# Performance work log

Hardware: AMD Instinct MI355X
Metric: run time of the kernel (lower is better)

## Reference

```python
import jax, jax.numpy as jnp
import numpy as np

D_MODEL = 256
D_STATE = 64
D_CONV = 4
EXPAND = 2
HEADDIM = 16
D_INNER = EXPAND * D_MODEL            # 512
NHEADS = D_INNER // HEADDIM           # 32
CONV_DIM = D_INNER + 2 * D_STATE      # 640 (ngroups=1)
D_IN_PROJ = 2 * D_INNER + 2 * D_STATE + NHEADS  # 1184
BATCH = 256
SEQ = 200


def _ln(x, g, b, eps=1e-12):
    m = jnp.mean(x, axis=-1, keepdims=True)
    v = jnp.mean((x - m) ** 2, axis=-1, keepdims=True)
    return (x - m) * jax.lax.rsqrt(v + eps) * g + b


def setup_inputs() -> dict:
    key = jax.random.key(0)
    ks = jax.random.split(key, 16)
    def gn(i, shape, s=0.02):
        return jax.random.normal(ks[i], shape, jnp.float32) * s
    return {
        "input_tensor": jax.random.normal(ks[0], (BATCH, SEQ, D_MODEL), jnp.float32),
        # Mamba2 params
        "in_proj_w": gn(1, (D_MODEL, D_IN_PROJ)),
        "conv_w": gn(2, (CONV_DIM, D_CONV), 0.1),
        "conv_b": jnp.zeros((CONV_DIM,), jnp.float32),
        "dt_bias": gn(3, (NHEADS,), 0.1),
        "A_log": jnp.log(jax.random.uniform(ks[4], (NHEADS,), jnp.float32, 1.0, 16.0)),
        "D_skip": jnp.ones((NHEADS,), jnp.float32),
        "rms_w": jnp.ones((D_INNER,), jnp.float32),
        "out_proj_w": gn(5, (D_INNER, D_MODEL)),
        # Layer norms / mixers
        "ln_g": jnp.ones((D_MODEL,), jnp.float32),
        "ln_b": jnp.zeros((D_MODEL,), jnp.float32),
        "filt_w": gn(6, (1, SEQ // 2 + 1, D_MODEL, 2), 0.02),
        "filt_ln_g": jnp.ones((D_MODEL,), jnp.float32),
        "filt_ln_b": jnp.zeros((D_MODEL,), jnp.float32),
        "alpha": jax.random.uniform(ks[7], (D_MODEL,), jnp.float32),
        "beta": jax.random.uniform(ks[8], (D_MODEL,), jnp.float32),
        # FFN
        "ffn_w1": gn(9, (D_MODEL, 4 * D_MODEL)),
        "ffn_b1": jnp.zeros((4 * D_MODEL,), jnp.float32),
        "ffn_w2": gn(10, (4 * D_MODEL, D_MODEL)),
        "ffn_b2": jnp.zeros((D_MODEL,), jnp.float32),
        "ffn_ln_g": jnp.ones((D_MODEL,), jnp.float32),
        "ffn_ln_b": jnp.zeros((D_MODEL,), jnp.float32),
    }


def _mamba2(x, in_proj_w, conv_w, conv_b, dt_bias, A_log, D_skip, rms_w, out_proj_w):
    b, l, _ = x.shape
    zxbcdt = x @ in_proj_w                                  # [b,l,1184]
    z, xBC, dt = jnp.split(zxbcdt, [D_INNER, D_INNER + CONV_DIM], axis=-1)
    # depthwise causal conv over time + SiLU
    xp = jnp.pad(xBC, ((0, 0), (D_CONV - 1, 0), (0, 0)))
    conv = conv_b + sum(conv_w[:, k] * xp[:, k:k + l, :] for k in range(D_CONV))
    xBC = jax.nn.silu(conv)
    xs, Bm, Cm = jnp.split(xBC, [D_INNER, D_INNER + D_STATE], axis=-1)
    xh = xs.reshape(b, l, NHEADS, HEADDIM)
    dt = jax.nn.softplus(dt + dt_bias)                      # [b,l,h]
    A = -jnp.exp(A_log)                                     # [h]
    dA = jnp.exp(dt * A)                                    # [b,l,h]
    dtx = dt[..., None] * xh                                # [b,l,h,p]

    def step(state, inp):
        dA_t, dtx_t, B_t, C_t = inp
        # state: [b,h,p,n]
        state = dA_t[:, :, None, None] * state + dtx_t[..., None] * B_t[:, None, None, :]
        y_t = jnp.einsum('bhpn,bn->bhp', state, C_t)
        return state, y_t

    state0 = jnp.zeros((b, NHEADS, HEADDIM, D_STATE), x.dtype)
    _, y = jax.lax.scan(step, state0,
                        (jnp.moveaxis(dA, 1, 0), jnp.moveaxis(dtx, 1, 0),
                         jnp.moveaxis(Bm, 1, 0), jnp.moveaxis(Cm, 1, 0)))
    y = jnp.moveaxis(y, 0, 1) + D_skip[None, None, :, None] * xh   # skip connection
    y = y.reshape(b, l, D_INNER)
    # gated RMSNorm: rmsnorm(y * silu(z)) * w
    g = y * jax.nn.silu(z)
    g = g * jax.lax.rsqrt(jnp.mean(g * g, axis=-1, keepdims=True) + 1e-5) * rms_w
    return g @ out_proj_w


def reference(input_tensor, in_proj_w, conv_w, conv_b, dt_bias, A_log, D_skip,
              rms_w, out_proj_w, ln_g, ln_b, filt_w, filt_ln_g, filt_ln_b,
              alpha, beta, ffn_w1, ffn_b1, ffn_w2, ffn_b2, ffn_ln_g, ffn_ln_b):
    x = input_tensor
    h1 = _mamba2(x, in_proj_w, conv_w, conv_b, dt_bias, A_log, D_skip, rms_w, out_proj_w)
    h1 = _ln(h1 + x, ln_g, ln_b)
    # FFT filter branch
    xf = jnp.fft.rfft(x, axis=1, norm='ortho')
    w = filt_w[..., 0] + 1j * filt_w[..., 1]                # [1,101,d]
    xi = jnp.fft.irfft(xf * w, n=SEQ, axis=1, norm='ortho').astype(x.dtype)
    h2 = _ln(xi + x, filt_ln_g, filt_ln_b)
    h = alpha * h1 + beta * h2
    hid = jax.nn.gelu(h @ ffn_w1 + ffn_b1, approximate=False) @ ffn_w2 + ffn_b2
    return _ln(hid + h, ffn_ln_g, ffn_ln_b)
```

## Files before the change

### kernel.cpp

```cpp
#include <hip/hip_runtime.h>
#include <math.h>

#define BATCHN 256
#define SEQ 200
#define DMODEL 256
#define DINNER 512
#define NH 32
#define HD 16
#define DSTATE 64
#define DINPROJ 1184
#define XBCLD 672
#define BL (BATCHN*SEQ)
#define NF 101
#define NJ 202
#define NJP 208
#define XBASE 655360
#define TC 25
#define NCH 8

typedef __attribute__((ext_vector_type(8))) short bf16x8;
typedef __attribute__((ext_vector_type(4))) float f32x4;

__device__ inline unsigned short f2bf(float f) {
    union { float f; unsigned u; } v; v.f = f;
    unsigned r = v.u + 0x7FFFu + ((v.u >> 16) & 1u);
    return (unsigned short)(r >> 16);
}
__device__ inline float bf2f(unsigned short h) {
    union { unsigned u; float f; } v; v.u = ((unsigned)h) << 16;
    return v.f;
}

#define GLOAD16(src, dst) __builtin_amdgcn_global_load_lds( \
    (const __attribute__((address_space(1))) void*)(src),   \
    (__attribute__((address_space(3))) void*)(dst), 16, 0, 0)

__global__ void init_dft_kernel(unsigned short* __restrict__ EF, unsigned short* __restrict__ EI)
{
    const float ang = 6.28318530717958647692f / 200.0f;
    int idx = blockIdx.x * 256 + threadIdx.x;
    if (idx < NJ * SEQ) {
        int f = idx / SEQ, t = idx - f * SEQ;
        float v;
        if (f <= 100) { int ph = (f * t) % 200; v = cosf(ang * (float)ph); }
        else { int ff = f - 101; int ph = (ff * t) % 200; v = -sinf(ang * (float)ph); }
        EF[idx] = f2bf(v);
    } else if (idx < NJ * SEQ + SEQ * NJP) {
        int j2 = idx - NJ * SEQ;
        int t = j2 / NJP, j = j2 - t * NJP;
        float v;
        if (j == 0) v = 1.0f / 200.0f;
        else if (j == 100) v = ((t & 1) ? -1.0f : 1.0f) / 200.0f;
        else if (j < 100) { int ph = (j * t) % 200; v = 2.0f * cosf(ang * (float)ph) / 200.0f; }
        else if (j >= 202 || j == 101 || j == 201) v = 0.0f;
        else { int f = j - 101; int ph = (f * t) % 200; v = -2.0f * sinf(ang * (float)ph) / 200.0f; }
        EI[j2] = f2bf(v);
    }
}

__global__ void pack_wT_kernel(const float* __restrict__ src, unsigned short* __restrict__ dst,
                               int srcld, int coloff, int N, int K)
{
    int idx = blockIdx.x * 256 + threadIdx.x;
    if (idx >= N * K) return;
    int n = idx / K, k = idx - n * K;
    dst[idx] = f2bf(src[(long long)k * srcld + coloff + n]);
}

__global__ void f2bf_kernel(const float* __restrict__ X, unsigned short* __restrict__ O)
{
    long long i = ((long long)blockIdx.x * 256 + threadIdx.x) * 8;
    float4 a = ((const float4*)(X + i))[0];
    float4 b = ((const float4*)(X + i))[1];
    uint4 o;
    o.x = (unsigned)f2bf(a.x) | ((unsigned)f2bf(a.y) << 16);
    o.y = (unsigned)f2bf(a.z) | ((unsigned)f2bf(a.w) << 16);
    o.z = (unsigned)f2bf(b.x) | ((unsigned)f2bf(b.y) << 16);
    o.w = (unsigned)f2bf(b.z) | ((unsigned)f2bf(b.w) << 16);
    *(uint4*)(O + i) = o;
}

__global__ void xT_kernel(const float* __restrict__ X, unsigned short* __restrict__ XT)
{
    __shared__ float tile[32][33];
    int b = blockIdx.z, t0 = blockIdx.x * 32, d0 = blockIdx.y * 32;
    int tx = threadIdx.x & 31, ty = threadIdx.x >> 5;
    const float* xb = X + (long long)b * SEQ * DMODEL;
#pragma unroll
    for (int i = 0; i < 4; i++) {
        int t = t0 + ty + i * 8;
        tile[ty + i * 8][tx] = (t < SEQ) ? xb[(long long)t * DMODEL + d0 + tx] : 0.f;
    }
    __syncthreads();
    unsigned short* xtb = XT + (long long)b * DMODEL * SEQ;
#pragma unroll
    for (int i = 0; i < 4; i++) {
        int d = d0 + ty + i * 8;
        int t = t0 + tx;
        if (t < SEQ) xtb[(long long)d * SEQ + t] = f2bf(tile[tx][ty + i * 8]);
    }
}

template<int ACT, int CBF>
__global__ __launch_bounds__(256) void mgemm_kernel(
    const unsigned short* __restrict__ Ab, const unsigned short* __restrict__ BTp,
    void* __restrict__ Cp, const float* __restrict__ bias,
    int M, int N, int K, int lda, int ldbt, int ldc,
    long long sA, long long sBT, long long sC)
{
    __shared__ unsigned short As[128 * 32];
    __shared__ unsigned short Bs[128 * 32];
    const unsigned short* Aa = Ab + (long long)blockIdx.z * sA;
    const unsigned short* Bt = BTp + (long long)blockIdx.z * sBT;
    float* Cf = (float*)Cp + (CBF ? 0 : (long long)blockIdx.z * sC);
    unsigned short* Cb = (unsigned short*)Cp + (CBF ? (long long)blockIdx.z * sC : 0);

    int m0 = blockIdx.y * 128, n0 = blockIdx.x * 128;
    int tid = threadIdx.x;
    int srow = tid >> 1, skb = (tid & 1) * 16;
    int w = tid >> 6, l = tid & 63;
    int wr = w >> 1, wc = w & 1;
    int fr = l & 15, fk = l >> 4;
    int glr = (w << 4) + (l >> 2);
    int glc = (l & 3) << 3;
    bool fullM = (m0 + 128 <= M);
    bool fullN = (n0 + 128 <= N);

    f32x4 acc[4][4] = {};

    for (int k0 = 0; k0 < K; k0 += 32) {
        bool kedge = (k0 + 32 > K);
        if (fullM && !kedge) {
            GLOAD16(Aa + (long long)(m0 + glr) * lda + k0 + glc,      &As[w << 9]);
            GLOAD16(Aa + (long long)(m0 + 64 + glr) * lda + k0 + glc, &As[2048 + (w << 9)]);
        } else {
            int gm = m0 + srow;
            unsigned short* dst = &As[srow * 32 + skb];
#pragma unroll
            for (int i = 0; i < 16; i++) {
                int gk = k0 + skb + i;
                dst[i] = (gm < M && gk < K) ? Aa[(long long)gm * lda + gk] : (unsigned short)0;
            }
        }
        if (fullN && !kedge) {
            GLOAD16(Bt + (long long)(n0 + glr) * ldbt + k0 + glc,      &Bs[w << 9]);
            GLOAD16(Bt + (long long)(n0 + 64 + glr) * ldbt + k0 + glc, &Bs[2048 + (w << 9)]);
        } else {
            int gn = n0 + srow;
            unsigned short* dst = &Bs[srow * 32 + skb];
#pragma unroll
            for (int i = 0; i < 16; i++) {
                int gk = k0 + skb + i;
                dst[i] = (gn < N && gk < K) ? Bt[(long long)gn * ldbt + gk] : (unsigned short)0;
            }
        }
        __syncthreads();
        bf16x8 a[4], b[4];
#pragma unroll
        for (int i = 0; i < 4; i++) {
            a[i] = *(const bf16x8*)&As[(wr * 64 + i * 16 + fr) * 32 + fk * 8];
            b[i] = *(const bf16x8*)&Bs[(wc * 64 + i * 16 + fr) * 32 + fk * 8];
        }
#pragma unroll
        for (int i = 0; i < 4; i++)
#pragma unroll
            for (int j = 0; j < 4; j++)
                acc[i][j] = __builtin_amdgcn_mfma_f32_16x16x32_bf16(a[i], b[j], acc[i][j], 0, 0, 0);
        __syncthreads();
    }

#pragma unroll
    for (int i = 0; i < 4; i++) {
        int gr0 = m0 + wr * 64 + i * 16 + fk * 4;
#pragma unroll
        for (int j = 0; j < 4; j++) {
            int gc = n0 + wc * 64 + j * 16 + fr;
            if (gc >= N) continue;
            float bv = bias ? bias[gc] : 0.f;
#pragma unroll
            for (int r = 0; r < 4; r++) {
                int gr = gr0 + r;
                if (gr >= M) continue;
                float v = acc[i][j][r] + bv;
                if (ACT == 1) v = 0.5f * v * (1.f + erff(v * 0.70710678118654752f));
                long long ci = (long long)gr * ldc + gc;
                if (CBF) Cb[ci] = f2bf(v);
                else Cf[ci] = v;
            }
        }
    }
}

__global__ void convbc_kernel(const float* __restrict__ XBC, const float* __restrict__ conv_w,
                              const float* __restrict__ conv_b, const float* __restrict__ dt_bias,
                              const float* __restrict__ A_log,
                              float* __restrict__ BCb, float* __restrict__ DTb, float* __restrict__ DAb)
{
    int row = blockIdx.x;
    int b = row / SEQ, l = row - b * SEQ;
    int tid = threadIdx.x;
    if (tid < 128) {
        int ch = 512 + tid;
        float acc = conv_b[ch];
#pragma unroll
        for (int k = 0; k < 4; k++) {
            int lt = l + k - 3;
            if (lt >= 0)
                acc = fmaf(conv_w[ch * 4 + k], XBC[(long long)(b * SEQ + lt) * XBCLD + ch], acc);
        }
        BCb[(long long)row * 128 + tid] = acc * __builtin_amdgcn_rcpf(1.f + __expf(-acc));
    } else if (tid < 160) {
        int h = tid - 128;
        float draw = XBC[(long long)row * XBCLD + 640 + h] + dt_bias[h];
        float dtv = (draw > 20.f) ? draw : log1pf(__expf(draw));
        DTb[(long long)row * NH + h] = dtv;
        DAb[(long long)row * NH + h] = __expf(-__expf(A_log[h]) * dtv);
    }
}

__device__ __forceinline__ void sstep(
    float raw, float dtv, float da,
    const float4& qb0, const float4& qb1, const float4& qb2, const float4& qb3,
    const float4& qc0, const float4& qc1, const float4& qc2, const float4& qc3,
    float cw0, float cw1, float cw2, float cw3, float cb, float ds,
    float* st, float& w0, float& w1, float& w2,
    int lane, float* __restrict__ yaddr)
{
    float cvv = cb + cw0 * w0 + cw1 * w1 + cw2 * w2 + cw3 * raw;
    float xhv = cvv * __builtin_amdgcn_rcpf(1.f + __expf(-cvv));
    w0 = w1; w1 = w2; w2 = raw;
    float xv = dtv * xhv;
    float p0, p1, p2, p3;
    st[0]  = fmaf(da, st[0],  xv * qb0.x); p0 = st[0]  * qc0.x;
    st[1]  = fmaf(da, st[1],  xv * qb0.y); p1 = st[1]  * qc0.y;
    st[2]  = fmaf(da, st[2],  xv * qb0.z); p2 = st[2]  * qc0.z;
    st[3]  = fmaf(da, st[3],  xv * qb0.w); p3 = st[3]  * qc0.w;
    st[4]  = fmaf(da, st[4],  xv * qb1.x); p0 = fmaf(st[4],  qc1.x, p0);
    st[5]  = fmaf(da, st[5],  xv * qb1.y); p1 = fmaf(st[5],  qc1.y, p1);
    st[6]  = fmaf(da, st[6],  xv * qb1.z); p2 = fmaf(st[6],  qc1.z, p2);
    st[7]  = fmaf(da, st[7],  xv * qb1.w); p3 = fmaf(st[7],  qc1.w, p3);
    st[8]  = fmaf(da, st[8],  xv * qb2.x); p0 = fmaf(st[8],  qc2.x, p0);
    st[9]  = fmaf(da, st[9],  xv * qb2.y); p1 = fmaf(st[9],  qc2.y, p1);
    st[10] = fmaf(da, st[10], xv * qb2.z); p2 = fmaf(st[10], qc2.z, p2);
    st[11] = fmaf(da, st[11], xv * qb2.w); p3 = fmaf(st[11], qc2.w, p3);
    st[12] = fmaf(da, st[12], xv * qb3.x); p0 = fmaf(st[12], qc3.x, p0);
    st[13] = fmaf(da, st[13], xv * qb3.y); p1 = fmaf(st[13], qc3.y, p1);
    st[14] = fmaf(da, st[14], xv * qb3.z); p2 = fmaf(st[14], qc3.z, p2);
    st[15] = fmaf(da, st[15], xv * qb3.w); p3 = fmaf(st[15], qc3.w, p3);
    float part = (p0 + p1) + (p2 + p3);
    part += __shfl_xor(part, 16);
    part += __shfl_xor(part, 32);
    if (lane < HD) *yaddr = part + ds * xhv;
}

__global__ __launch_bounds__(256) void scan6_kernel(
    const float* __restrict__ DTb, const float* __restrict__ DAb,
    float* __restrict__ XBC, const float* __restrict__ BCb,
    const float* __restrict__ Dsk,
    const float* __restrict__ conv_w, const float* __restrict__ conv_b)
{
    __shared__ float sbc[2][TC][128];
    __shared__ unsigned short sx[2][TC][128];
    __shared__ float sdt[SEQ][8];
    __shared__ float sda[SEQ][8];
    int tid = threadIdx.x;
    int wv = tid >> 6, lane = tid & 63;
    int bid = blockIdx.x;
    int b = bid >> 2, hq = (bid & 3) * 8;
    long long rowb = (long long)b * SEQ;

    for (int i = tid; i < SEQ * 8; i += 256) {
        int t = i >> 3, j = i & 7;
        sdt[t][j] = DTb[(rowb + t) * NH + hq + j];
        sda[t][j] = DAb[(rowb + t) * NH + hq + j];
    }
    for (int i = tid; i < TC * 32; i += 256) {
        int r = i >> 5, c = i & 31;
        ((float4*)&sbc[0][r][0])[c] = ((const float4*)(BCb + (rowb + r) * 128))[c];
    }
    for (int i = tid; i < TC * 64; i += 256) {
        int r = i >> 6, c2 = i & 63;
        float2 v = *(const float2*)(XBC + (rowb + r) * XBCLD + hq * 16 + (c2 << 1));
        *(unsigned*)&sx[0][r][c2 << 1] = (unsigned)f2bf(v.x) | ((unsigned)f2bf(v.y) << 16);
    }
    __syncthreads();

    int p = lane & 15, g = lane >> 4;
    int hA = hq + wv, hB = hq + 4 + wv;
    int chA = hA * HD + p, chB = hB * HD + p;
    float cwA0 = conv_w[chA * 4 + 0], cwA1 = conv_w[chA * 4 + 1];
    float cwA2 = conv_w[chA * 4 + 2], cwA3 = conv_w[chA * 4 + 3];
    float cbA = conv_b[chA];
    float cwB0 = conv_w[chB * 4 + 0], cwB1 = conv_w[chB * 4 + 1];
    float cwB2 = conv_w[chB * 4 + 2], cwB3 = conv_w[chB * 4 + 3];
    float cbB = conv_b[chB];
    float dsA = Dsk[hA], dsB = Dsk[hB];
    int xcA = wv * 16 + p, xcB = (4 + wv) * 16 + p;
    float* ypA = XBC + rowb * XBCLD + hA * HD + p;
    float* ypB = XBC + rowb * XBCLD + hB * HD + p;
    float stA[16], stB[16];
#pragma unroll
    for (int r = 0; r < 16; r++) { stA[r] = 0.f; stB[r] = 0.f; }
    float wA0 = 0.f, wA1 = 0.f, wA2 = 0.f;
    float wB0 = 0.f, wB1 = 0.f, wB2 = 0.f;

    for (int c = 0; c < NCH; c++) {
        int cur = c & 1;
        if (c + 1 < NCH) {
            int nb = cur ^ 1;
            long long tb = rowb + (c + 1) * TC;
            for (int i = tid; i < TC * 32; i += 256) {
                int r = i >> 5, cc = i & 31;
                ((float4*)&sbc[nb][r][0])[cc] = ((const float4*)(BCb + (tb + r) * 128))[cc];
            }
            for (int i = tid; i < TC * 64; i += 256) {
                int r = i >> 6, c2 = i & 63;
                float2 v = *(const float2*)(XBC + (tb + r) * XBCLD + hq * 16 + (c2 << 1));
                *(unsigned*)&sx[nb][r][c2 << 1] = (unsigned)f2bf(v.x) | ((unsigned)f2bf(v.y) << 16);
            }
        }
        int tbase = c * TC;
        for (int t = 0; t < TC; t++) {
            int gt = tbase + t;
            const float4* qb = (const float4*)&sbc[cur][t][g * 16];
            const float4* qc = (const float4*)&sbc[cur][t][64 + g * 16];
            float4 qb0 = qb[0], qb1 = qb[1], qb2 = qb[2], qb3 = qb[3];
            float4 qc0 = qc[0], qc1 = qc[1], qc2 = qc[2], qc3 = qc[3];
            float rawA = bf2f(sx[cur][t][xcA]);
            float rawB = bf2f(sx[cur][t][xcB]);
            sstep(rawA, sdt[gt][wv], sda[gt][wv], qb0, qb1, qb2, qb3, qc0, qc1, qc2, qc3,
                  cwA0, cwA1, cwA2, cwA3, cbA, dsA, stA, wA0, wA1, wA2,
                  lane, ypA + (long long)gt * XBCLD);
            sstep(rawB, sdt[gt][4 + wv], sda[gt][4 + wv], qb0, qb1, qb2, qb3, qc0, qc1, qc2, qc3,
                  cwB0, cwB1, cwB2, cwB3, cbB, dsB, stB, wB0, wB1, wB2,
                  lane, ypB + (long long)gt * XBCLD);
        }
        __syncthreads();
    }
}

__global__ __launch_bounds__(256) void gate_kernel(
    float* __restrict__ XBC, const unsigned short* __restrict__ Zbf,
    const float* __restrict__ rms_w)
{
    int row = blockIdx.x * 4 + (threadIdx.x >> 6);
    int lane = threadIdx.x & 63;
    float* yrow = XBC + (long long)row * XBCLD + lane * 8;
    const unsigned short* zrow = Zbf + (long long)row * 512 + lane * 8;
    float4 y0 = ((const float4*)yrow)[0];
    float4 y1 = ((const float4*)yrow)[1];
    uint4 zq = ((const uint4*)zrow)[0];
    float yv[8] = { y0.x, y0.y, y0.z, y0.w, y1.x, y1.y, y1.z, y1.w };
    float zv[8];
    zv[0] = bf2f((unsigned short)(zq.x & 0xFFFF)); zv[1] = bf2f((unsigned short)(zq.x >> 16));
    zv[2] = bf2f((unsigned short)(zq.y & 0xFFFF)); zv[3] = bf2f((unsigned short)(zq.y >> 16));
    zv[4] = bf2f((unsigned short)(zq.z & 0xFFFF)); zv[5] = bf2f((unsigned short)(zq.z >> 16));
    zv[6] = bf2f((unsigned short)(zq.w & 0xFFFF)); zv[7] = bf2f((unsigned short)(zq.w >> 16));
    float a[8]; float ss = 0.f;
#pragma unroll
    for (int i = 0; i < 8; i++) {
        float z = zv[i];
        a[i] = yv[i] * (z * __builtin_amdgcn_rcpf(1.f + __expf(-z)));
        ss = fmaf(a[i], a[i], ss);
    }
#pragma unroll
    for (int m = 1; m < 64; m <<= 1) ss += __shfl_xor(ss, m);
    float sc = rsqrtf(ss * (1.f / 512.f) + 1e-5f);
    const float* rw = rms_w + lane * 8;
    float4 r0 = ((const float4*)rw)[0];
    float4 r1 = ((const float4*)rw)[1];
    float rv[8] = { r0.x, r0.y, r0.z, r0.w, r1.x, r1.y, r1.z, r1.w };
    uint4 o;
    o.x = (unsigned)f2bf(a[0] * sc * rv[0]) | ((unsigned)f2bf(a[1] * sc * rv[1]) << 16);
    o.y = (unsigned)f2bf(a[2] * sc * rv[2]) | ((unsigned)f2bf(a[3] * sc * rv[3]) << 16);
    o.z = (unsigned)f2bf(a[4] * sc * rv[4]) | ((unsigned)f2bf(a[5] * sc * rv[5]) << 16);
    o.w = (unsigned)f2bf(a[6] * sc * rv[6]) | ((unsigned)f2bf(a[7] * sc * rv[7]) << 16);
    unsigned short* grow = (unsigned short*)(XBC + (long long)row * XBCLD);
    ((uint4*)grow)[lane] = o;
}

__global__ void lnadd_kernel(const float* __restrict__ A, const float* __restrict__ Bb,
                             const float* __restrict__ g, const float* __restrict__ be,
                             float* __restrict__ O)
{
    int row = blockIdx.x * 4 + (threadIdx.x >> 6);
    int lane = threadIdx.x & 63;
    long long base = (long long)row * DMODEL + lane * 4;
    float v[4]; float s1 = 0.f;
#pragma unroll
    for (int i = 0; i < 4; i++) { float a = A[base + i] + Bb[base + i]; v[i] = a; s1 += a; }
#pragma unroll
    for (int m = 1; m < 64; m <<= 1) s1 += __shfl_xor(s1, m);
    float mean = s1 * (1.f / 256.f);
    float s2 = 0.f;
#pragma unroll
    for (int i = 0; i < 4; i++) { float d = v[i] - mean; s2 = fmaf(d, d, s2); }
#pragma unroll
    for (int m = 1; m < 64; m <<= 1) s2 += __shfl_xor(s2, m);
    float r = rsqrtf(s2 * (1.f / 256.f) + 1e-12f);
#pragma unroll
    for (int i = 0; i < 4; i++)
        O[base + i] = (v[i] - mean) * r * g[lane * 4 + i] + be[lane * 4 + i];
}

__global__ void lnadd_bf_kernel(const unsigned short* __restrict__ A, const float* __restrict__ Bb,
                                const float* __restrict__ g, const float* __restrict__ be,
                                float* __restrict__ O)
{
    int row = blockIdx.x * 4 + (threadIdx.x >> 6);
    int lane = threadIdx.x & 63;
    long long base = (long long)row * DMODEL + lane * 4;
    float v[4]; float s1 = 0.f;
#pragma unroll
    for (int i = 0; i < 4; i++) { float a = bf2f(A[base + i]) + Bb[base + i]; v[i] = a; s1 += a; }
#pragma unroll
    for (int m = 1; m < 64; m <<= 1) s1 += __shfl_xor(s1, m);
    float mean = s1 * (1.f / 256.f);
    float s2 = 0.f;
#pragma unroll
    for (int i = 0; i < 4; i++) { float d = v[i] - mean; s2 = fmaf(d, d, s2); }
#pragma unroll
    for (int m = 1; m < 64; m <<= 1) s2 += __shfl_xor(s2, m);
    float r = rsqrtf(s2 * (1.f / 256.f) + 1e-12f);
#pragma unroll
    for (int i = 0; i < 4; i++)
        O[base + i] = (v[i] - mean) * r * g[lane * 4 + i] + be[lane * 4 + i];
}

__global__ void combine_kernel(const float* __restrict__ XI, const float* __restrict__ X,
                               float* __restrict__ H1, unsigned short* __restrict__ HB,
                               const float* __restrict__ fg, const float* __restrict__ fb,
                               const float* __restrict__ al, const float* __restrict__ bt)
{
    int row = blockIdx.x * 4 + (threadIdx.x >> 6);
    int lane = threadIdx.x & 63;
    long long base = (long long)row * DMODEL + lane * 4;
    float v[4]; float s1 = 0.f;
#pragma unroll
    for (int i = 0; i < 4; i++) { float a = XI[base + i] + X[base + i]; v[i] = a; s1 += a; }
#pragma unroll
    for (int m = 1; m < 64; m <<= 1) s1 += __shfl_xor(s1, m);
    float mean = s1 * (1.f / 256.f);
    float s2 = 0.f;
#pragma unroll
    for (int i = 0; i < 4; i++) { float d = v[i] - mean; s2 = fmaf(d, d, s2); }
#pragma unroll
    for (int m = 1; m < 64; m <<= 1) s2 += __shfl_xor(s2, m);
    float r = rsqrtf(s2 * (1.f / 256.f) + 1e-12f);
#pragma unroll
    for (int i = 0; i < 4; i++) {
        float h2 = (v[i] - mean) * r * fg[lane * 4 + i] + fb[lane * 4 + i];
        float h = al[lane * 4 + i] * H1[base + i] + bt[lane * 4 + i] * h2;
        H1[base + i] = h;
        HB[base + i] = f2bf(h);
    }
}

__global__ void filt_kernel(unsigned short* __restrict__ XF, const float* __restrict__ W)
{
    long long idx = (long long)blockIdx.x * 256 + threadIdx.x;
    if (idx >= (long long)BATCHN * DMODEL * NF) return;
    int f = (int)(idx % NF);
    int d = (int)((idx / NF) % DMODEL);
    int b = (int)(idx / ((long long)NF * DMODEL));
    long long base = ((long long)b * DMODEL + d) * NJP;
    float re = bf2f(XF[base + f]);
    float im = bf2f(XF[base + 101 + f]);
    float wr = W[((long long)f * DMODEL + d) * 2];
    float wi = W[((long long)f * DMODEL + d) * 2 + 1];
    XF[base + f]       = f2bf(re * wr - im * wi);
    XF[base + 101 + f] = f2bf(re * wi + im * wr);
}

extern "C" void kernel_launch(void* const* d_in, const int* in_sizes, int n_in,
                              void* d_out, int out_size, void* d_ws, size_t ws_size,
                              hipStream_t stream)
{
    const float* x          = (const float*)d_in[0];
    const float* in_proj_w  = (const float*)d_in[1];
    const float* conv_w     = (const float*)d_in[2];
    const float* conv_b     = (const float*)d_in[3];
    const float* dt_bias    = (const float*)d_in[4];
    const float* A_log      = (const float*)d_in[5];
    const float* D_skip     = (const float*)d_in[6];
    const float* rms_w      = (const float*)d_in[7];
    const float* out_proj_w = (const float*)d_in[8];
    const float* ln_g       = (const float*)d_in[9];
    const float* ln_b       = (const float*)d_in[10];
    const float* filt_w     = (const float*)d_in[11];
    const float* filt_ln_g  = (const float*)d_in[12];
    const float* filt_ln_b  = (const float*)d_in[13];
    const float* alpha      = (const float*)d_in[14];
    const float* beta       = (const float*)d_in[15];
    const float* ffn_w1     = (const float*)d_in[16];
    const float* ffn_b1     = (const float*)d_in[17];
    const float* ffn_w2     = (const float*)d_in[18];
    const float* ffn_b2     = (const float*)d_in[19];
    const float* ffn_ln_g   = (const float*)d_in[20];
    const float* ffn_ln_b   = (const float*)d_in[21];
    float* out = (float*)d_out;
    float* ws = (float*)d_ws;

    unsigned short* WP   = (unsigned short*)(ws + 81920);
    unsigned short* ipwT = WP;
    unsigned short* opwT = ipwT + 672 * 256;
    unsigned short* w1T  = opwT + 256 * 512;
    unsigned short* w2T  = w1T + 1024 * 256;
    unsigned short* zwT  = w2T + 256 * 1024;
    unsigned short* EFbf = zwT + 512 * 256;
    unsigned short* EIbf = EFbf + NJ * SEQ;
    float* XBC = ws + XBASE;
    float* BCb = XBC + (long long)BL * XBCLD;
    float* DTb = BCb + (long long)BL * 128;
    float* DAb = DTb + (long long)BL * NH;
    float* MO  = DAb + (long long)BL * NH;
    unsigned short* Zbf = (unsigned short*)MO;
    unsigned short* xbf  = (unsigned short*)BCb;
    unsigned short* xTbf = (unsigned short*)BCb;
    unsigned short* MObf = (unsigned short*)BCb;
    unsigned short* Gbf = (unsigned short*)XBC;
    unsigned short* XFT = (unsigned short*)XBC;
    float* XI  = XBC + 7000000;
    unsigned short* HID = (unsigned short*)XBC;
    unsigned short* FFO = (unsigned short*)(XBC + 26500000);

    init_dft_kernel<<<dim3((NJ * SEQ + SEQ * NJP + 255) / 256), dim3(256), 0, stream>>>(EFbf, EIbf);
    pack_wT_kernel<<<dim3((672 * 256 + 255) / 256), dim3(256), 0, stream>>>(in_proj_w, ipwT, DINPROJ, 512, 672, 256);
    pack_wT_kernel<<<dim3((512 * 256 + 255) / 256), dim3(256), 0, stream>>>(in_proj_w, zwT, DINPROJ, 0, 512, 256);
    pack_wT_kernel<<<dim3((256 * 512 + 255) / 256), dim3(256), 0, stream>>>(out_proj_w, opwT, 256, 0, 256, 512);
    pack_wT_kernel<<<dim3((1024 * 256 + 255) / 256), dim3(256), 0, stream>>>(ffn_w1, w1T, 1024, 0, 1024, 256);
    pack_wT_kernel<<<dim3((256 * 1024 + 255) / 256), dim3(256), 0, stream>>>(ffn_w2, w2T, 256, 0, 256, 1024);
    f2bf_kernel<<<dim3(BL * DMODEL / 2048), dim3(256), 0, stream>>>(x, xbf);

    mgemm_kernel<0,0><<<dim3(6, BL / 128, 1), dim3(256), 0, stream>>>(
        xbf, ipwT, XBC, nullptr, BL, 672, 256, 256, 256, 672, 0, 0, 0);

    mgemm_kernel<0,1><<<dim3(4, BL / 128, 1), dim3(256), 0, stream>>>(
        xbf, zwT, Zbf, nullptr, BL, 512, 256, 256, 256, 512, 0, 0, 0);

    convbc_kernel<<<dim3(BL), dim3(192), 0, stream>>>(XBC, conv_w, conv_b, dt_bias, A_log,
                                                      BCb, DTb, DAb);

    scan6_kernel<<<dim3(BATCHN * 4), dim3(256), 0, stream>>>(DTb, DAb, XBC, BCb, D_skip,
                                                             conv_w, conv_b);

    xT_kernel<<<dim3(7, 8, BATCHN), dim3(256), 0, stream>>>(x, xTbf);

    gate_kernel<<<dim3(BL / 4), dim3(256), 0, stream>>>(XBC, Zbf, rms_w);

    mgemm_kernel<0,0><<<dim3(2, BL / 128, 1), dim3(256), 0, stream>>>(
        Gbf, opwT, MO, nullptr, BL, 256, 512, 1344, 512, 256, 0, 0, 0);

    lnadd_kernel<<<dim3(BL / 4), dim3(256), 0, stream>>>(MO, x, ln_g, ln_b, MO);

    mgemm_kernel<0,1><<<dim3(2, 2, BATCHN), dim3(256), 0, stream>>>(
        xTbf, EFbf, XFT, nullptr, 256, NJ, SEQ, SEQ, SEQ, NJP,
        (long long)DMODEL * SEQ, 0, (long long)DMODEL * NJP);

    filt_kernel<<<dim3((BATCHN * DMODEL * NF + 255) / 256), dim3(256), 0, stream>>>(XFT, filt_w);

    mgemm_kernel<0,0><<<dim3(2, 2, BATCHN), dim3(256), 0, stream>>>(
        EIbf, XFT, XI, nullptr, SEQ, DMODEL, NJ, NJP, NJP, DMODEL,
        0, (long long)DMODEL * NJP, (long long)SEQ * DMODEL);

    combine_kernel<<<dim3(BL / 4), dim3(256), 0, stream>>>(XI, x, MO, MObf,
                                                           filt_ln_g, filt_ln_b, alpha, beta);

    mgemm_kernel<1,1><<<dim3(8, BL / 128, 1), dim3(256), 0, stream>>>(
        MObf, w1T, HID, ffn_b1, BL, 1024, 256, 256, 256, 1024, 0, 0, 0);

    mgemm_kernel<0,1><<<dim3(2, BL / 128, 1), dim3(256), 0, stream>>>(
        HID, w2T, FFO, ffn_b2, BL, 256, 1024, 1024, 1024, 256, 0, 0, 0);

    lnadd_bf_kernel<<<dim3(BL / 4), dim3(256), 0, stream>>>(FFO, MO, ffn_ln_g, ffn_ln_b, out);
}
```

Measured before the change: 970.5 us.

## Fuse mamba residual LayerNorm into combine, pad DFT GEMMs, chunk-stream dt in scan

Removes the separate lnadd pass over the mamba output by computing both LayerNorms (mamba residual and FFT-filter branch) inside a single combine2 kernel. The DFT basis matrices and spectrum buffers are zero-padded to 256 so the batched forward and inverse DFT GEMMs use aligned full tiles with no ragged edges. The scan kernel now double-buffers dt and dA per time chunk with a smaller chunk size, which shrinks shared memory and may allow more resident blocks. In exchange the padded GEMMs do extra multiply-adds on zero rows and columns, and the scan takes more chunk barriers.

```diff
diff --git a/kernel.cpp b/kernel.cpp
--- a/kernel.cpp
+++ b/kernel.cpp
@@ -13,10 +13,10 @@
 #define BL (BATCHN*SEQ)
 #define NF 101
 #define NJ 202
-#define NJP 208
 #define XBASE 655360
-#define TC 25
-#define NCH 8
+#define TC 20
+#define NCH 10
+#define XIOFF 8500000
 
 typedef __attribute__((ext_vector_type(8))) short bf16x8;
 typedef __attribute__((ext_vector_type(4))) float f32x4;
@@ -39,17 +39,19 @@
 {
     const float ang = 6.28318530717958647692f / 200.0f;
     int idx = blockIdx.x * 256 + threadIdx.x;
-    if (idx < NJ * SEQ) {
+    if (idx < 256 * SEQ) {
         int f = idx / SEQ, t = idx - f * SEQ;
         float v;
         if (f <= 100) { int ph = (f * t) % 200; v = cosf(ang * (float)ph); }
-        else { int ff = f - 101; int ph = (ff * t) % 200; v = -sinf(ang * (float)ph); }
+        else if (f <= 201) { int ff = f - 101; int ph = (ff * t) % 200; v = -sinf(ang * (float)ph); }
+        else v = 0.f;
         EF[idx] = f2bf(v);
-    } else if (idx < NJ * SEQ + SEQ * NJP) {
-        int j2 = idx - NJ * SEQ;
-        int t = j2 / NJP, j = j2 - t * NJP;
+    } else if (idx < 256 * SEQ + 256 * 256) {
+        int j2 = idx - 256 * SEQ;
+        int t = j2 >> 8, j = j2 & 255;
         float v;
-        if (j == 0) v = 1.0f / 200.0f;
+        if (t >= 200) v = 0.f;
+        else if (j == 0) v = 1.0f / 200.0f;
         else if (j == 100) v = ((t & 1) ? -1.0f : 1.0f) / 200.0f;
         else if (j < 100) { int ph = (j * t) % 200; v = 2.0f * cosf(ang * (float)ph) / 200.0f; }
         else if (j >= 202 || j == 101 || j == 201) v = 0.0f;
@@ -253,7 +255,7 @@
     if (lane < HD) *yaddr = part + ds * xhv;
 }
 
-__global__ __launch_bounds__(256) void scan6_kernel(
+__global__ __launch_bounds__(256) void scan7_kernel(
     const float* __restrict__ DTb, const float* __restrict__ DAb,
     float* __restrict__ XBC, const float* __restrict__ BCb,
     const float* __restrict__ Dsk,
@@ -261,19 +263,14 @@
 {
     __shared__ float sbc[2][TC][128];
     __shared__ unsigned short sx[2][TC][128];
-    __shared__ float sdt[SEQ][8];
-    __shared__ float sda[SEQ][8];
+    __shared__ float sdt[2][TC][8];
+    __shared__ float sda[2][TC][8];
     int tid = threadIdx.x;
     int wv = tid >> 6, lane = tid & 63;
     int bid = blockIdx.x;
     int b = bid >> 2, hq = (bid & 3) * 8;
     long long rowb = (long long)b * SEQ;
 
-    for (int i = tid; i < SEQ * 8; i += 256) {
-        int t = i >> 3, j = i & 7;
-        sdt[t][j] = DTb[(rowb + t) * NH + hq + j];
-        sda[t][j] = DAb[(rowb + t) * NH + hq + j];
-    }
     for (int i = tid; i < TC * 32; i += 256) {
         int r = i >> 5, c = i & 31;
         ((float4*)&sbc[0][r][0])[c] = ((const float4*)(BCb + (rowb + r) * 128))[c];
@@ -282,6 +279,11 @@
         int r = i >> 6, c2 = i & 63;
         float2 v = *(const float2*)(XBC + (rowb + r) * XBCLD + hq * 16 + (c2 << 1));
         *(unsigned*)&sx[0][r][c2 << 1] = (unsigned)f2bf(v.x) | ((unsigned)f2bf(v.y) << 16);
+    }
+    for (int i = tid; i < TC * 8; i += 256) {
+        int t = i >> 3, j = i & 7;
+        sdt[0][t][j] = DTb[(rowb + t) * NH + hq + j];
+        sda[0][t][j] = DAb[(rowb + t) * NH + hq + j];
     }
     __syncthreads();
 
@@ -318,6 +320,11 @@
                 float2 v = *(const float2*)(XBC + (tb + r) * XBCLD + hq * 16 + (c2 << 1));
                 *(unsigned*)&sx[nb][r][c2 << 1] = (unsigned)f2bf(v.x) | ((unsigned)f2bf(v.y) << 16);
             }
+            for (int i = tid; i < TC * 8; i += 256) {
+                int t = i >> 3, j = i & 7;
+                sdt[nb][t][j] = DTb[(tb + t) * NH + hq + j];
+                sda[nb][t][j] = DAb[(tb + t) * NH + hq + j];
+            }
         }
         int tbase = c * TC;
         for (int t = 0; t < TC; t++) {
@@ -328,10 +335,10 @@
             float4 qc0 = qc[0], qc1 = qc[1], qc2 = qc[2], qc3 = qc[3];
             float rawA = bf2f(sx[cur][t][xcA]);
             float rawB = bf2f(sx[cur][t][xcB]);
-            sstep(rawA, sdt[gt][wv], sda[gt][wv], qb0, qb1, qb2, qb3, qc0, qc1, qc2, qc3,
+            sstep(rawA, sdt[cur][t][wv], sda[cur][t][wv], qb0, qb1, qb2, qb3, qc0, qc1, qc2, qc3,
                   cwA0, cwA1, cwA2, cwA3, cbA, dsA, stA, wA0, wA1, wA2,
                   lane, ypA + (long long)gt * XBCLD);
-            sstep(rawB, sdt[gt][4 + wv], sda[gt][4 + wv], qb0, qb1, qb2, qb3, qc0, qc1, qc2, qc3,
+            sstep(rawB, sdt[cur][t][4 + wv], sda[cur][t][4 + wv], qb0, qb1, qb2, qb3, qc0, qc1, qc2, qc3,
                   cwB0, cwB1, cwB2, cwB3, cbB, dsB, stB, wB0, wB1, wB2,
                   lane, ypB + (long long)gt * XBCLD);
         }
@@ -379,16 +386,16 @@
     ((uint4*)grow)[lane] = o;
 }
 
-__global__ void lnadd_kernel(const float* __restrict__ A, const float* __restrict__ Bb,
-                             const float* __restrict__ g, const float* __restrict__ be,
-                             float* __restrict__ O)
+__global__ void lnadd_bf_kernel(const unsigned short* __restrict__ A, const float* __restrict__ Bb,
+                                const float* __restrict__ g, const float* __restrict__ be,
+                                float* __restrict__ O)
 {
     int row = blockIdx.x * 4 + (threadIdx.x >> 6);
     int lane = threadIdx.x & 63;
     long long base = (long long)row * DMODEL + lane * 4;
     float v[4]; float s1 = 0.f;
 #pragma unroll
-    for (int i = 0; i < 4; i++) { float a = A[base + i] + Bb[base + i]; v[i] = a; s1 += a; }
+    for (int i = 0; i < 4; i++) { float a = bf2f(A[base + i]) + Bb[base + i]; v[i] = a; s1 += a; }
 #pragma unroll
     for (int m = 1; m < 64; m <<= 1) s1 += __shfl_xor(s1, m);
     float mean = s1 * (1.f / 256.f);
@@ -403,55 +410,45 @@
         O[base + i] = (v[i] - mean) * r * g[lane * 4 + i] + be[lane * 4 + i];
 }
 
-__global__ void lnadd_bf_kernel(const unsigned short* __restrict__ A, const float* __restrict__ Bb,
-                                const float* __restrict__ g, const float* __restrict__ be,
-                                float* __restrict__ O)
+__global__ void combine2_kernel(const float* __restrict__ XI, const float* __restrict__ X,
+                                float* __restrict__ MO, unsigned short* __restrict__ HB,
+                                const float* __restrict__ lg, const float* __restrict__ lb,
+                                const float* __restrict__ fg, const float* __restrict__ fb,
+                                const float* __restrict__ al, const float* __restrict__ bt)
 {
     int row = blockIdx.x * 4 + (threadIdx.x >> 6);
     int lane = threadIdx.x & 63;
     long long base = (long long)row * DMODEL + lane * 4;
-    float v[4]; float s1 = 0.f;
-#pragma unroll
-    for (int i = 0; i < 4; i++) { float a = bf2f(A[base + i]) + Bb[base + i]; v[i] = a; s1 += a; }
-#pragma unroll
-    for (int m = 1; m < 64; m <<= 1) s1 += __shfl_xor(s1, m);
-    float mean = s1 * (1.f / 256.f);
-    float s2 = 0.f;
-#pragma unroll
-    for (int i = 0; i < 4; i++) { float d = v[i] - mean; s2 = fmaf(d, d, s2); }
-#pragma unroll
-    for (int m = 1; m < 64; m <<= 1) s2 += __shfl_xor(s2, m);
-    float r = rsqrtf(s2 * (1.f / 256.f) + 1e-12f);
-#pragma unroll
-    for (int i = 0; i < 4; i++)
-        O[base + i] = (v[i] - mean) * r * g[lane * 4 + i] + be[lane * 4 + i];
-}
-
-__global__ void combine_kernel(const float* __restrict__ XI, const float* __restrict__ X,
-                               float* __restrict__ H1, unsigned short* __restrict__ HB,
-                               const float* __restrict__ fg, const float* __restrict__ fb,
-                               const float* __restrict__ al, const float* __restrict__ bt)
-{
-    int row = blockIdx.x * 4 + (threadIdx.x >> 6);
-    int lane = threadIdx.x & 63;
-    long long base = (long long)row * DMODEL + lane * 4;
-    float v[4]; float s1 = 0.f;
-#pragma unroll
-    for (int i = 0; i < 4; i++) { float a = XI[base + i] + X[base + i]; v[i] = a; s1 += a; }
-#pragma unroll
-    for (int m = 1; m < 64; m <<= 1) s1 += __shfl_xor(s1, m);
-    float mean = s1 * (1.f / 256.f);
-    float s2 = 0.f;
-#pragma unroll
-    for (int i = 0; i < 4; i++) { float d = v[i] - mean; s2 = fmaf(d, d, s2); }
-#pragma unroll
-    for (int m = 1; m < 64; m <<= 1) s2 += __shfl_xor(s2, m);
-    float r = rsqrtf(s2 * (1.f / 256.f) + 1e-12f);
+    int bb = row / SEQ, ll = row - bb * SEQ;
+    long long xib = (long long)bb * 65536 + ll * 256 + lane * 4;
+    float u[4], v[4]; float su = 0.f, sv = 0.f;
 #pragma unroll
     for (int i = 0; i < 4; i++) {
-        float h2 = (v[i] - mean) * r * fg[lane * 4 + i] + fb[lane * 4 + i];
-        float h = al[lane * 4 + i] * H1[base + i] + bt[lane * 4 + i] * h2;
-        H1[base + i] = h;
+        float xv = X[base + i];
+        float a = MO[base + i] + xv;
+        float b = XI[xib + i] + xv;
+        u[i] = a; v[i] = b; su += a; sv += b;
+    }
+#pragma unroll
+    for (int m = 1; m < 64; m <<= 1) { su += __shfl_xor(su, m); sv += __shfl_xor(sv, m); }
+    float mu = su * (1.f / 256.f), mv = sv * (1.f / 256.f);
+    float qu = 0.f, qv = 0.f;
+#pragma unroll
+    for (int i = 0; i < 4; i++) {
+        float du = u[i] - mu; qu = fmaf(du, du, qu);
+        float dv = v[i] - mv; qv = fmaf(dv, dv, qv);
+    }
+#pragma unroll
+    for (int m = 1; m < 64; m <<= 1) { qu += __shfl_xor(qu, m); qv += __shfl_xor(qv, m); }
+    float ru = rsqrtf(qu * (1.f / 256.f) + 1e-12f);
+    float rv = rsqrtf(qv * (1.f / 256.f) + 1e-12f);
+#pragma unroll
+    for (int i = 0; i < 4; i++) {
+        int d = lane * 4 + i;
+        float h1 = (u[i] - mu) * ru * lg[d] + lb[d];
+        float h2 = (v[i] - mv) * rv * fg[d] + fb[d];
+        float h = al[d] * h1 + bt[d] * h2;
+        MO[base + i] = h;
         HB[base + i] = f2bf(h);
     }
 }
@@ -463,7 +460,7 @@
     int f = (int)(idx % NF);
     int d = (int)((idx / NF) % DMODEL);
     int b = (int)(idx / ((long long)NF * DMODEL));
-    long long base = ((long long)b * DMODEL + d) * NJP;
+    long long base = ((long long)b * DMODEL + d) * 256;
     float re = bf2f(XF[base + f]);
     float im = bf2f(XF[base + 101 + f]);
     float wr = W[((long long)f * DMODEL + d) * 2];
@@ -508,7 +505,7 @@
     unsigned short* w2T  = w1T + 1024 * 256;
     unsigned short* zwT  = w2T + 256 * 1024;
     unsigned short* EFbf = zwT + 512 * 256;
-    unsigned short* EIbf = EFbf + NJ * SEQ;
+    unsigned short* EIbf = EFbf + 256 * SEQ;
     float* XBC = ws + XBASE;
     float* BCb = XBC + (long long)BL * XBCLD;
     float* DTb = BCb + (long long)BL * 128;
@@ -520,11 +517,11 @@
     unsigned short* MObf = (unsigned short*)BCb;
     unsigned short* Gbf = (unsigned short*)XBC;
     unsigned short* XFT = (unsigned short*)XBC;
-    float* XI  = XBC + 7000000;
+    float* XI  = XBC + XIOFF;
     unsigned short* HID = (unsigned short*)XBC;
     unsigned short* FFO = (unsigned short*)(XBC + 26500000);
 
-    init_dft_kernel<<<dim3((NJ * SEQ + SEQ * NJP + 255) / 256), dim3(256), 0, stream>>>(EFbf, EIbf);
+    init_dft_kernel<<<dim3((256 * SEQ + 256 * 256 + 255) / 256), dim3(256), 0, stream>>>(EFbf, EIbf);
     pack_wT_kernel<<<dim3((672 * 256 + 255) / 256), dim3(256), 0, stream>>>(in_proj_w, ipwT, DINPROJ, 512, 672, 256);
     pack_wT_kernel<<<dim3((512 * 256 + 255) / 256), dim3(256), 0, stream>>>(in_proj_w, zwT, DINPROJ, 0, 512, 256);
     pack_wT_kernel<<<dim3((256 * 512 + 255) / 256), dim3(256), 0, stream>>>(out_proj_w, opwT, 256, 0, 256, 512);
@@ -541,7 +538,7 @@
     convbc_kernel<<<dim3(BL), dim3(192), 0, stream>>>(XBC, conv_w, conv_b, dt_bias, A_log,
                                                       BCb, DTb, DAb);
 
-    scan6_kernel<<<dim3(BATCHN * 4), dim3(256), 0, stream>>>(DTb, DAb, XBC, BCb, D_skip,
+    scan7_kernel<<<dim3(BATCHN * 4), dim3(256), 0, stream>>>(DTb, DAb, XBC, BCb, D_skip,
                                                              conv_w, conv_b);
 
     xT_kernel<<<dim3(7, 8, BATCHN), dim3(256), 0, stream>>>(x, xTbf);
@@ -551,20 +548,19 @@
     mgemm_kernel<0,0><<<dim3(2, BL / 128, 1), dim3(256), 0, stream>>>(
         Gbf, opwT, MO, nullptr, BL, 256, 512, 1344, 512, 256, 0, 0, 0);
 
-    lnadd_kernel<<<dim3(BL / 4), dim3(256), 0, stream>>>(MO, x, ln_g, ln_b, MO);
-
     mgemm_kernel<0,1><<<dim3(2, 2, BATCHN), dim3(256), 0, stream>>>(
-        xTbf, EFbf, XFT, nullptr, 256, NJ, SEQ, SEQ, SEQ, NJP,
-        (long long)DMODEL * SEQ, 0, (long long)DMODEL * NJP);
+        xTbf, EFbf, XFT, nullptr, 256, 256, SEQ, SEQ, SEQ, 256,
+        (long long)DMODEL * SEQ, 0, 65536);
 
     filt_kernel<<<dim3((BATCHN * DMODEL * NF + 255) / 256), dim3(256), 0, stream>>>(XFT, filt_w);
 
     mgemm_kernel<0,0><<<dim3(2, 2, BATCHN), dim3(256), 0, stream>>>(
-        EIbf, XFT, XI, nullptr, SEQ, DMODEL, NJ, NJP, NJP, DMODEL,
-        0, (long long)DMODEL * NJP, (long long)SEQ * DMODEL);
-
-    combine_kernel<<<dim3(BL / 4), dim3(256), 0, stream>>>(XI, x, MO, MObf,
-                                                           filt_ln_g, filt_ln_b, alpha, beta);
+        EIbf, XFT, XI, nullptr, 256, 256, 256, 256, 256, 256,
+        0, 65536, 65536);
+
+    combine2_kernel<<<dim3(BL / 4), dim3(256), 0, stream>>>(XI, x, MO, MObf,
+                                                            ln_g, ln_b, filt_ln_g, filt_ln_b,
+                                                            alpha, beta);
 
     mgemm_kernel<1,1><<<dim3(8, BL / 128, 1), dim3(256), 0, stream>>>(
         MObf, w1T, HID, ffn_b1, BL, 1024, 256, 256, 256, 1024, 0, 0, 0);
```

Result: faster. 859.9 us (-11.4%).
